# Kernel tuning notes

Measured on AMD Instinct MI355X. Metric: run time of the kernel, lower is better.

Reference implementation:

```python
import jax, jax.numpy as jnp
import numpy as np

N_NODES = 4096
N_EDGES = 32768
IN_FEAT = 256
OUT_FEAT = 128
HID = 64
IN_HEAD = 64
OUT_HEAD = 5
NEG_SLOPE = 0.2
EPS = 1e-16


def setup_inputs() -> dict:
    key = jax.random.key(0)
    ks = jax.random.split(key, 12)
    x = jax.random.normal(ks[0], (N_NODES, IN_FEAT), dtype=jnp.float32)
    src = jax.random.randint(ks[1], (N_EDGES,), 0, N_NODES)
    dst = jax.random.randint(ks[2], (N_EDGES,), 0, N_NODES)
    edge_index = jnp.stack([src, dst]).astype(jnp.int64)
    s1 = 1.0 / np.sqrt(IN_FEAT)
    s2 = 1.0 / np.sqrt(HID * IN_HEAD)
    W1 = jax.random.normal(ks[3], (IN_FEAT, IN_HEAD * HID), dtype=jnp.float32) * s1
    att_src1 = jax.random.normal(ks[4], (IN_HEAD, HID), dtype=jnp.float32) * 0.1
    att_dst1 = jax.random.normal(ks[5], (IN_HEAD, HID), dtype=jnp.float32) * 0.1
    b1 = jnp.zeros((IN_HEAD * HID,), dtype=jnp.float32)
    W2 = jax.random.normal(ks[6], (IN_HEAD * HID, OUT_HEAD * OUT_FEAT), dtype=jnp.float32) * s2
    att_src2 = jax.random.normal(ks[7], (OUT_HEAD, OUT_FEAT), dtype=jnp.float32) * 0.1
    att_dst2 = jax.random.normal(ks[8], (OUT_HEAD, OUT_FEAT), dtype=jnp.float32) * 0.1
    b2 = jnp.zeros((OUT_FEAT,), dtype=jnp.float32)
    return {"x": x, "edge_index": edge_index, "W1": W1, "att_src1": att_src1,
            "att_dst1": att_dst1, "b1": b1, "W2": W2, "att_src2": att_src2,
            "att_dst2": att_dst2, "b2": b2}


def _gat_conv(x, W, att_src, att_dst, bias, src, dst, heads, out_c, concat):
    # x: [N, F_in]; returns [N, heads*out_c] (concat) or [N, out_c] (mean)
    n = x.shape[0]
    h = (x @ W).reshape(n, heads, out_c)                       # [N,H,C]
    a_src = jnp.sum(h * att_src, axis=-1)                      # [N,H]
    a_dst = jnp.sum(h * att_dst, axis=-1)                      # [N,H]
    e = jax.nn.leaky_relu(a_src[src] + a_dst[dst], NEG_SLOPE)  # [E,H]
    # segment softmax over edges grouped by destination node (PyG softmax)
    m = jax.ops.segment_max(e, dst, num_segments=n)            # [N,H]
    ex = jnp.exp(e - m[dst])
    denom = jax.ops.segment_sum(ex, dst, num_segments=n)       # [N,H]
    alpha = ex / (denom[dst] + EPS)                            # [E,H]
    out = jax.ops.segment_sum(alpha[:, :, None] * h[src], dst, num_segments=n)  # [N,H,C]
    out = out.reshape(n, heads * out_c) if concat else out.mean(axis=1)
    return out + bias


def reference(x, edge_index, W1, att_src1, att_dst1, b1, W2, att_src2, att_dst2, b2):
    n = x.shape[0]
    # PyG GATConv default: add self loops
    loop = jnp.arange(n, dtype=edge_index.dtype)
    src = jnp.concatenate([edge_index[0], loop])
    dst = jnp.concatenate([edge_index[1], loop])
    # dropout layers are identity in eval mode
    h = _gat_conv(x, W1, att_src1, att_dst1, b1, src, dst, IN_HEAD, HID, True)
    h = jax.nn.elu(h)
    h = _gat_conv(h, W2, att_src2, att_dst2, b2, src, dst, OUT_HEAD, OUT_FEAT, False)
    s = jnp.mean(h, axis=0)
    return jnp.tanh(s)
```

## Files before the change

kernel.cpp:

```cpp
#include <hip/hip_runtime.h>
#include <hip/hip_bf16.h>

#define N_NODES 4096
#define NE      32768
#define E_TOT   (NE + N_NODES)
#define IN_FEAT 256
#define HID     64
#define IN_HEAD 64
#define F1      4096
#define OUT_HEAD 5
#define OUT_FEAT 128
#define F2      640
#define NEG_SLOPE 0.2f
#define EPS_A   1e-16f

typedef __bf16 bf16;
typedef bf16 bf16x8 __attribute__((ext_vector_type(8)));
typedef bf16 bf16x4 __attribute__((ext_vector_type(4)));
typedef float f32x4 __attribute__((ext_vector_type(4)));

__device__ inline void async_cp16(bf16* lds, const bf16* g) {
    __builtin_amdgcn_global_load_lds(
        (const __attribute__((address_space(1))) unsigned int*)g,
        (__attribute__((address_space(3))) unsigned int*)lds, 16, 0, 0);
}

__global__ void scan_kernel(const int* __restrict__ counts,
                            int* __restrict__ row_start, int* __restrict__ cursor) {
    __shared__ int part[256];
    __shared__ int pre[257];
    int t = threadIdx.x;
    int base = t * 16;
    int local[16];
    int s = 0;
#pragma unroll
    for (int i = 0; i < 16; ++i) { local[i] = s; s += counts[base + i]; }
    part[t] = s;
    __syncthreads();
    if (t == 0) {
        int r = 0;
        for (int i = 0; i < 256; ++i) { pre[i] = r; r += part[i]; }
        pre[256] = r;
    }
    __syncthreads();
    int off = pre[t];
#pragma unroll
    for (int i = 0; i < 16; ++i) {
        int v = off + local[i];
        row_start[base + i] = v;
        cursor[base + i] = v;
    }
    if (t == 0) row_start[N_NODES] = pre[256];
}

__global__ void scatter_kernel(const int* __restrict__ esrc,
                               const int* __restrict__ edst,
                               int* cursor, int* __restrict__ srclist) {
    int e = blockIdx.x * 256 + threadIdx.x;
    if (e >= E_TOT) return;
    int d = (e < NE) ? edst[e] : (e - NE);
    int s = (e < NE) ? esrc[e] : (e - NE);
    int slot = atomicAdd(&cursor[d], 1);
    srclist[slot] = s;
}

#define PB_X   512
#define PB_W1  1024
#define PB_W2  2560
#define PB_ATT 64
#define PB_TOT (PB_X + PB_W1 + PB_W2 + PB_ATT)
#define PB_HIST 144
__global__ __launch_bounds__(256)
void prep_kernel(const float* __restrict__ x, bf16* __restrict__ xb,
                 const float* __restrict__ W1, bf16* __restrict__ W1T,
                 const float* __restrict__ W2, bf16* __restrict__ W2T,
                 const float* __restrict__ as1, const float* __restrict__ ad1,
                 bf16* __restrict__ w1s, bf16* __restrict__ w1d,
                 const int* __restrict__ edst, int* __restrict__ counts) {
    __shared__ float tile[32][33];
    int b = blockIdx.x, t = threadIdx.x;
    if (b < PB_X) {
        int i = b * 256 + t;
        f32x4 a = *(const f32x4*)(x + (size_t)i * 8);
        f32x4 c = *(const f32x4*)(x + (size_t)i * 8 + 4);
        bf16x8 r;
        r[0] = (bf16)a[0]; r[1] = (bf16)a[1]; r[2] = (bf16)a[2]; r[3] = (bf16)a[3];
        r[4] = (bf16)c[0]; r[5] = (bf16)c[1]; r[6] = (bf16)c[2]; r[7] = (bf16)c[3];
        *(bf16x8*)(xb + (size_t)i * 8) = r;
    } else if (b < PB_X + PB_W1 + PB_W2) {
        const float* S; bf16* D; int R, C, gx, gy;
        if (b < PB_X + PB_W1) {
            int bb = b - PB_X;
            S = W1; D = W1T; R = IN_FEAT; C = F1;
            gx = bb % (F1 / 32); gy = bb / (F1 / 32);
        } else {
            int bb = b - PB_X - PB_W1;
            S = W2; D = W2T; R = F1; C = F2;
            gx = bb % (F2 / 32); gy = bb / (F2 / 32);
        }
        int tx = t & 31, ty = t >> 5;
        int c0 = gx * 32, r0 = gy * 32;
#pragma unroll
        for (int i = 0; i < 4; ++i)
            tile[ty + i * 8][tx] = S[(size_t)(r0 + ty + i * 8) * C + c0 + tx];
        __syncthreads();
#pragma unroll
        for (int i = 0; i < 4; ++i)
            D[(size_t)(c0 + ty + i * 8) * R + r0 + tx] = (bf16)tile[tx][ty + i * 8];
    } else if (b < PB_TOT) {
        int id = (b - PB_X - PB_W1 - PB_W2) * 256 + t;
        int k = id >> 6, h = id & 63;
        const float* wrow = W1 + (size_t)k * F1 + h * HID;
        const float* a1 = as1 + h * HID;
        const float* a2 = ad1 + h * HID;
        float s = 0.f, d = 0.f;
#pragma unroll 8
        for (int c = 0; c < HID; ++c) {
            float w = wrow[c];
            s += w * a1[c];
            d += w * a2[c];
        }
        w1s[id] = (bf16)s;
        w1d[id] = (bf16)d;
    } else {
        int e = (b - PB_TOT) * 256 + t;
        if (e < E_TOT) {
            int d = (e < NE) ? edst[e] : (e - NE);
            atomicAdd(&counts[d], 1);
        }
    }
}

template <int SPLITK, typename TC>
__device__ __forceinline__
void gemm_body(const bf16* __restrict__ A, const bf16* __restrict__ BT,
               TC* __restrict__ C, int M, int N, int K,
               int nb, int mb, int zb) {
    __shared__ bf16 As[128][64];
    __shared__ bf16 Bs[128][64];
    const int tid  = threadIdx.x;
    const int wave = tid >> 6, lane = tid & 63;
    const int quad = lane >> 4, lr = lane & 15;
    const int m0 = mb * 128, n0 = nb * 128;
    const int kchunk = K / SPLITK;
    const int kbeg = zb * kchunk;
    const int wm = (wave >> 1) * 64;
    const int wn = (wave & 1) * 64;
    TC* Cz = C + (size_t)zb * M * N;

    const int srow = lane >> 3;
    const int scol = ((lane & 7) ^ srow) * 8;
    const int xk = lr & 7;

    f32x4 acc[4][4] = {};

    for (int kk = 0; kk < kchunk; kk += 64) {
        int k0 = kbeg + kk;
#pragma unroll
        for (int c = 0; c < 4; ++c) {
            int r = wave * 32 + c * 8;
            async_cp16(&As[r][0], A + (size_t)(m0 + r + srow) * K + k0 + scol);
            async_cp16(&Bs[r][0], BT + (size_t)(n0 + r + srow) * K + k0 + scol);
        }
        __syncthreads();

#pragma unroll
        for (int ks = 0; ks < 2; ++ks) {
            int ch = ((ks * 4 + quad) ^ xk) * 8;
            bf16x8 af[4], bfr[4];
#pragma unroll
            for (int mt = 0; mt < 4; ++mt)
                af[mt] = *(const bf16x8*)(&As[wm + mt * 16 + lr][ch]);
#pragma unroll
            for (int nt = 0; nt < 4; ++nt)
                bfr[nt] = *(const bf16x8*)(&Bs[wn + nt * 16 + lr][ch]);
#pragma unroll
            for (int mt = 0; mt < 4; ++mt)
#pragma unroll
                for (int nt = 0; nt < 4; ++nt)
                    acc[mt][nt] = __builtin_amdgcn_mfma_f32_16x16x32_bf16(
                        af[mt], bfr[nt], acc[mt][nt], 0, 0, 0);
        }
        __syncthreads();
    }

#pragma unroll
    for (int mt = 0; mt < 4; ++mt)
#pragma unroll
        for (int nt = 0; nt < 4; ++nt) {
            int row0 = m0 + wm + mt * 16 + quad * 4;
            int col = n0 + wn + nt * 16 + lr;
#pragma unroll
            for (int r = 0; r < 4; ++r)
                Cz[(size_t)(row0 + r) * N + col] = (TC)acc[mt][nt][r];
        }
}

__global__ __launch_bounds__(256)
void gemm2_kernel(const bf16* __restrict__ A, const bf16* __restrict__ BT,
                  bf16* __restrict__ C) {
    int bid = blockIdx.x;
    int xx = bid & 7, q = bid >> 3;
    int gp = q / 5; int nb = q - gp * 5;
    int g = gp * 8 + xx;
    int mb = g >> 2, zb = g & 3;
    gemm_body<4, bf16>(A, BT, C, N_NODES, F2, F1, nb, mb, zb);
}

__global__ __launch_bounds__(256)
void layer1_kernel(const bf16* __restrict__ xb, const bf16* __restrict__ W1T,
                   bf16* __restrict__ H1,
                   const float* __restrict__ x,
                   const bf16* __restrict__ w1s, const bf16* __restrict__ w1d,
                   float* __restrict__ a_src, float* __restrict__ a_dst) {
    int bid = blockIdx.x;
    if (bid < 1024) {
        gemm_body<1, bf16>(xb, W1T, H1, N_NODES, F1, IN_FEAT,
                           bid & 31, bid >> 5, 0);
    } else {
        int wave = threadIdx.x >> 6, lane = threadIdx.x & 63;
        int n = (bid - 1024) * 4 + wave;
        const float* xr = x + (size_t)n * IN_FEAT;
        float s = 0.f, d = 0.f;
        for (int k0 = 0; k0 < IN_FEAT; k0 += 4) {
            f32x4 xv = *(const f32x4*)(xr + k0);
#pragma unroll
            for (int j = 0; j < 4; ++j) {
                float xs = xv[j];
                s += xs * (float)w1s[(k0 + j) * IN_HEAD + lane];
                d += xs * (float)w1d[(k0 + j) * IN_HEAD + lane];
            }
        }
        a_src[n * IN_HEAD + lane] = s;
        a_dst[n * IN_HEAD + lane] = d;
    }
}

__global__ __launch_bounds__(64)
void agg1_kernel(const int* __restrict__ row_start,
                 const int* __restrict__ srclist,
                 const float* __restrict__ a_src, const float* __restrict__ a_dst,
                 const bf16* __restrict__ H1, const float* __restrict__ b1,
                 bf16* __restrict__ h_elu) {
    int bid = blockIdx.x;
    int c = bid & 7;
    int d = bid >> 3;
    int lane = threadIdx.x;
    int gh = c * 8 + (lane >> 3);
    int beg = row_start[d], deg = row_start[d + 1] - beg;
    float adst = a_dst[d * IN_HEAD + gh];
    int fbase = c * 512 + lane * 8;
    const float* asg = a_src + gh;

    auto SL = [&](int i) { return srclist[beg + (i < deg ? i : deg - 1)]; };

    int s0 = SL(0), s1 = SL(1), s2 = SL(2), s3 = SL(3);
    float la0 = asg[(size_t)s0 * IN_HEAD];
    bf16x8 v0 = *(const bf16x8*)(H1 + (size_t)s0 * F1 + fbase);
    float la1 = asg[(size_t)s1 * IN_HEAD];
    bf16x8 v1 = *(const bf16x8*)(H1 + (size_t)s1 * F1 + fbase);
    float la2 = asg[(size_t)s2 * IN_HEAD];
    bf16x8 v2 = *(const bf16x8*)(H1 + (size_t)s2 * F1 + fbase);
    float la3 = asg[(size_t)s3 * IN_HEAD];
    bf16x8 v3 = *(const bf16x8*)(H1 + (size_t)s3 * F1 + fbase);
    int s4 = SL(4), s5 = SL(5);

    float m = -1e30f, den = 0.f;
    float acc[8] = {};
    for (int i = 0; i < deg; ++i) {
        int sn = SL(i + 6);
        float la4 = asg[(size_t)s4 * IN_HEAD];
        bf16x8 v4 = *(const bf16x8*)(H1 + (size_t)s4 * F1 + fbase);

        float l = la0 + adst;
        l = l > 0.f ? l : NEG_SLOPE * l;
        if (l > m + 12.f) {
            float r = __expf(m - l);
            den *= r;
#pragma unroll
            for (int k = 0; k < 8; ++k) acc[k] *= r;
            m = l;
        }
        float w = __expf(l - m);
        den += w;
#pragma unroll
        for (int k = 0; k < 8; ++k) acc[k] += w * (float)v0[k];

        la0 = la1; v0 = v1;
        la1 = la2; v1 = v2;
        la2 = la3; v2 = v3;
        la3 = la4; v3 = v4;
        s4 = s5; s5 = sn;
    }
    float dinv = 1.f / (den + EPS_A);

    bf16x8 o;
#pragma unroll
    for (int j = 0; j < 8; ++j) {
        float v = acc[j] * dinv + b1[fbase + j];
        o[j] = (bf16)(v > 0.f ? v : (__expf(v) - 1.f));
    }
    *(bf16x8*)(h_elu + (size_t)d * F1 + fbase) = o;
}

__global__ __launch_bounds__(192)
void fold2_kernel(const bf16* __restrict__ Hp,
                  const float* __restrict__ as2, const float* __restrict__ ad2,
                  float* __restrict__ H2,
                  float* __restrict__ a_src, float* __restrict__ a_dst) {
    int n = blockIdx.x, t = threadIdx.x;
    if (t >= 160) return;
    int h = t >> 5;
    f32x4 sum = {};
#pragma unroll
    for (int z = 0; z < 4; ++z) {
        bf16x4 v = *(const bf16x4*)(Hp + (size_t)z * N_NODES * F2 + (size_t)n * F2 + t * 4);
        sum[0] += (float)v[0]; sum[1] += (float)v[1];
        sum[2] += (float)v[2]; sum[3] += (float)v[3];
    }
    *(f32x4*)(H2 + (size_t)n * F2 + t * 4) = sum;
    f32x4 ws = *(const f32x4*)(as2 + t * 4);
    f32x4 wd = *(const f32x4*)(ad2 + t * 4);
    float s = sum[0] * ws[0] + sum[1] * ws[1] + sum[2] * ws[2] + sum[3] * ws[3];
    float d = sum[0] * wd[0] + sum[1] * wd[1] + sum[2] * wd[2] + sum[3] * wd[3];
#pragma unroll
    for (int o = 1; o <= 16; o <<= 1) {
        s += __shfl_xor(s, o);
        d += __shfl_xor(d, o);
    }
    if ((t & 31) == 0) {
        a_src[n * OUT_HEAD + h] = s;
        a_dst[n * OUT_HEAD + h] = d;
    }
}

__global__ void stats2_kernel(const int* __restrict__ row_start,
                              const int* __restrict__ srclist,
                              const float* __restrict__ a_src,
                              const float* __restrict__ a_dst,
                              float* __restrict__ m2, float* __restrict__ dinv2,
                              float* __restrict__ beta) {
    int id = blockIdx.x * 256 + threadIdx.x;
    if (id >= N_NODES * OUT_HEAD) return;
    beta[id] = 0.f;
    int d = id / OUT_HEAD, h = id - d * OUT_HEAD;
    int beg = row_start[d], deg = row_start[d + 1] - beg;
    float adst = a_dst[id];
    auto SL = [&](int i) { return srclist[beg + (i < deg ? i : deg - 1)]; };
    int s0 = SL(0), s1 = SL(1);
    float la0 = a_src[s0 * OUT_HEAD + h];
    float m = -1e30f, den = 0.f;
    for (int i = 0; i < deg; ++i) {
        int s2 = SL(i + 2);
        float la1 = a_src[s1 * OUT_HEAD + h];
        float l = la0 + adst;
        l = l > 0.f ? l : NEG_SLOPE * l;
        if (l > m + 12.f) { den *= __expf(m - l); m = l; }
        den += __expf(l - m);
        la0 = la1; s1 = s2;
    }
    m2[id] = m;
    dinv2[id] = 1.f / (den + EPS_A);
}

__global__ void beta_kernel(const int* __restrict__ es, const int* __restrict__ ed,
                            const float* __restrict__ a_src, const float* __restrict__ a_dst,
                            const float* __restrict__ m2, const float* __restrict__ dinv2,
                            float* __restrict__ beta,
                            float* __restrict__ acc_out, int* __restrict__ ticket) {
    int id = blockIdx.x * 256 + threadIdx.x;
    if (id < 8 * OUT_FEAT) acc_out[id] = 0.f;
    else if (id == 8 * OUT_FEAT) *ticket = 0;
    if (id >= E_TOT * OUT_HEAD) return;
    int e = id / OUT_HEAD, h = id - e * OUT_HEAD;
    int s = (e < NE) ? es[e] : (e - NE);
    int d = (e < NE) ? ed[e] : (e - NE);
    float l = a_src[s * OUT_HEAD + h] + a_dst[d * OUT_HEAD + h];
    l = l > 0.f ? l : NEG_SLOPE * l;
    float alpha = __expf(l - m2[d * OUT_HEAD + h]) * dinv2[d * OUT_HEAD + h];
    atomicAdd(&beta[s * OUT_HEAD + h], alpha);
}

__global__ __launch_bounds__(256)
void wsum_kernel(const float* __restrict__ H2, const float* __restrict__ beta,
                 float* __restrict__ acc_out, const float* __restrict__ b2,
                 float* __restrict__ out, int* __restrict__ ticket) {
    __shared__ float buf[F2];
    __shared__ int lastblk;
    int t = threadIdx.x;
    int n0 = blockIdx.x * 32;
    int h = t >> 5;
    float a0 = 0.f, a1 = 0.f, a2 = 0.f, a3 = 0.f;
    if (t < 160) {
        for (int i = 0; i < 32; ++i) {
            int s = n0 + i;
            float bh = beta[s * OUT_HEAD + h];
            f32x4 v = *(const f32x4*)(H2 + (size_t)s * F2 + t * 4);
            a0 += bh * v[0]; a1 += bh * v[1];
            a2 += bh * v[2]; a3 += bh * v[3];
        }
        buf[t * 4 + 0] = a0; buf[t * 4 + 1] = a1;
        buf[t * 4 + 2] = a2; buf[t * 4 + 3] = a3;
    }
    __syncthreads();
    if (t < OUT_FEAT) {
        float s = 0.f;
#pragma unroll
        for (int hh = 0; hh < OUT_HEAD; ++hh) s += buf[hh * OUT_FEAT + t];
        atomicAdd(&acc_out[(blockIdx.x & 7) * OUT_FEAT + t], s);
    }
    __syncthreads();
    if (t == 0) {
        __threadfence();
        lastblk = (atomicAdd(ticket, 1) == (int)gridDim.x - 1);
    }
    __syncthreads();
    if (lastblk && t < OUT_FEAT) {
        float tot = 0.f;
#pragma unroll
        for (int k = 0; k < 8; ++k)
            tot += atomicAdd(&acc_out[k * OUT_FEAT + t], 0.0f);
        out[t] = tanhf(tot * (1.f / (OUT_HEAD * (float)N_NODES)) + b2[t]);
    }
}

extern "C" void kernel_launch(void* const* d_in, const int* in_sizes, int n_in,
                              void* d_out, int out_size, void* d_ws, size_t ws_size,
                              hipStream_t stream) {
    const float* x        = (const float*)d_in[0];
    const int*   ei       = (const int*)d_in[1];
    const float* W1       = (const float*)d_in[2];
    const float* att_src1 = (const float*)d_in[3];
    const float* att_dst1 = (const float*)d_in[4];
    const float* b1       = (const float*)d_in[5];
    const float* W2       = (const float*)d_in[6];
    const float* att_src2 = (const float*)d_in[7];
    const float* att_dst2 = (const float*)d_in[8];
    const float* b2       = (const float*)d_in[9];
    float* out = (float*)d_out;

    const int* esrc = ei;
    const int* edst = ei + NE;

    char* p = (char*)d_ws;
    auto bump = [&](size_t bytes) {
        void* r = (void*)p;
        p += (bytes + 255) & ~(size_t)255;
        return r;
    };
    bf16*  H1     = (bf16*)bump((size_t)N_NODES * F1 * 2);
    bf16*  h_elu  = (bf16*)bump((size_t)N_NODES * F1 * 2);
    bf16*  Hp     = (bf16*)bump((size_t)4 * N_NODES * F2 * 2);
    float* H2     = (float*)bump((size_t)N_NODES * F2 * 4);
    bf16*  xb     = (bf16*)bump((size_t)N_NODES * IN_FEAT * 2);
    bf16*  W1T    = (bf16*)bump((size_t)F1 * IN_FEAT * 2);
    bf16*  W2T    = (bf16*)bump((size_t)F2 * F1 * 2);
    bf16*  w1s    = (bf16*)bump((size_t)IN_FEAT * IN_HEAD * 2);
    bf16*  w1d    = (bf16*)bump((size_t)IN_FEAT * IN_HEAD * 2);
    float* a_src1 = (float*)bump((size_t)N_NODES * IN_HEAD * 4);
    float* a_dst1 = (float*)bump((size_t)N_NODES * IN_HEAD * 4);
    float* a_src2 = (float*)bump((size_t)N_NODES * OUT_HEAD * 4);
    float* a_dst2 = (float*)bump((size_t)N_NODES * OUT_HEAD * 4);
    float* m2     = (float*)bump((size_t)N_NODES * OUT_HEAD * 4);
    float* dinv2  = (float*)bump((size_t)N_NODES * OUT_HEAD * 4);
    int*   row_start = (int*)bump((N_NODES + 1) * 4);
    int*   cursor  = (int*)bump(N_NODES * 4);
    int*   srclist = (int*)bump(E_TOT * 4);
    int*   counts  = (int*)bump(N_NODES * 4);
    float* beta    = (float*)bump((size_t)N_NODES * OUT_HEAD * 4);
    float* acc_out = (float*)bump((size_t)8 * OUT_FEAT * 4);
    int*   ticket  = (int*)bump(4);

    hipMemsetAsync(counts, 0, N_NODES * 4, stream);
    prep_kernel<<<PB_TOT + PB_HIST, 256, 0, stream>>>(
        x, xb, W1, W1T, W2, W2T, att_src1, att_dst1, w1s, w1d, edst, counts);
    scan_kernel<<<1, 256, 0, stream>>>(counts, row_start, cursor);
    scatter_kernel<<<(E_TOT + 255) / 256, 256, 0, stream>>>(
        esrc, edst, cursor, srclist);

    layer1_kernel<<<2048, 256, 0, stream>>>(
        xb, W1T, H1, x, w1s, w1d, a_src1, a_dst1);
    agg1_kernel<<<N_NODES * 8, 64, 0, stream>>>(
        row_start, srclist, a_src1, a_dst1, H1, b1, h_elu);

    gemm2_kernel<<<640, 256, 0, stream>>>(h_elu, W2T, Hp);
    fold2_kernel<<<N_NODES, 192, 0, stream>>>(
        Hp, att_src2, att_dst2, H2, a_src2, a_dst2);
    stats2_kernel<<<(N_NODES * OUT_HEAD + 255) / 256, 256, 0, stream>>>(
        row_start, srclist, a_src2, a_dst2, m2, dinv2, beta);
    beta_kernel<<<(E_TOT * OUT_HEAD + 255) / 256, 256, 0, stream>>>(
        esrc, edst, a_src2, a_dst2, m2, dinv2, beta, acc_out, ticket);
    wsum_kernel<<<N_NODES / 32, 256, 0, stream>>>(
        H2, beta, acc_out, b2, out, ticket);
}
```

Baseline: 238.7 us.

## Split layer-1 GEMM and GEMV into separate kernels with wider GEMM tile

The fused layer1 kernel, which mixed GEMM blocks with attention-logit GEMV blocks, is split into a dedicated gemm1 kernel and a separate gemv1 kernel. The new GEMM uses a 128x256 output tile per block (8 N-subtiles per wave) on a 2D grid, which doubles reuse of the A tile and halves the number of blocks. The wider tile raises accumulator register pressure and LDS use, and adds one more kernel launch. The shared gemm_body template is inlined into each kernel.

Result: slower. 251.3 us (+5.3%).

```diff
diff --git a/kernel.cpp b/kernel.cpp
--- a/kernel.cpp
+++ b/kernel.cpp
@@ -131,109 +131,158 @@
     }
 }
 
-template <int SPLITK, typename TC>
-__device__ __forceinline__
-void gemm_body(const bf16* __restrict__ A, const bf16* __restrict__ BT,
-               TC* __restrict__ C, int M, int N, int K,
-               int nb, int mb, int zb) {
+__global__ __launch_bounds__(256)
+void gemm1_kernel(const bf16* __restrict__ A, const bf16* __restrict__ BT,
+                  bf16* __restrict__ C) {
+    __shared__ bf16 As[128][64];
+    __shared__ bf16 Bs[256][64];
+    const int tid  = threadIdx.x;
+    const int wave = tid >> 6, lane = tid & 63;
+    const int quad = lane >> 4, lr = lane & 15;
+    const int nb = blockIdx.x;
+    const int mb = blockIdx.y;
+    const int m0 = mb * 128, n0 = nb * 256;
+    const int wm = (wave >> 1) * 64;
+    const int wn = (wave & 1) * 128;
+
+    const int srow = lane >> 3;
+    const int scol = ((lane & 7) ^ srow) * 8;
+    const int xk = lr & 7;
+
+    f32x4 acc[4][8] = {};
+
+    for (int k0 = 0; k0 < IN_FEAT; k0 += 64) {
+#pragma unroll
+        for (int c = 0; c < 4; ++c) {
+            int r = wave * 32 + c * 8;
+            async_cp16(&As[r][0], A + (size_t)(m0 + r + srow) * IN_FEAT + k0 + scol);
+        }
+#pragma unroll
+        for (int c = 0; c < 8; ++c) {
+            int r = wave * 64 + c * 8;
+            async_cp16(&Bs[r][0], BT + (size_t)(n0 + r + srow) * IN_FEAT + k0 + scol);
+        }
+        __syncthreads();
+
+#pragma unroll
+        for (int ks = 0; ks < 2; ++ks) {
+            int ch = ((ks * 4 + quad) ^ xk) * 8;
+            bf16x8 af[4], bfr[8];
+#pragma unroll
+            for (int mt = 0; mt < 4; ++mt)
+                af[mt] = *(const bf16x8*)(&As[wm + mt * 16 + lr][ch]);
+#pragma unroll
+            for (int nt = 0; nt < 8; ++nt)
+                bfr[nt] = *(const bf16x8*)(&Bs[wn + nt * 16 + lr][ch]);
+#pragma unroll
+            for (int mt = 0; mt < 4; ++mt)
+#pragma unroll
+                for (int nt = 0; nt < 8; ++nt)
+                    acc[mt][nt] = __builtin_amdgcn_mfma_f32_16x16x32_bf16(
+                        af[mt], bfr[nt], acc[mt][nt], 0, 0, 0);
+        }
+        __syncthreads();
+    }
+
+#pragma unroll
+    for (int mt = 0; mt < 4; ++mt)
+#pragma unroll
+        for (int nt = 0; nt < 8; ++nt) {
+            int row0 = m0 + wm + mt * 16 + quad * 4;
+            int col = n0 + wn + nt * 16 + lr;
+#pragma unroll
+            for (int r = 0; r < 4; ++r)
+                C[(size_t)(row0 + r) * F1 + col] = (bf16)acc[mt][nt][r];
+        }
+}
+
+__global__ __launch_bounds__(256)
+void gemm2_kernel(const bf16* __restrict__ A, const bf16* __restrict__ BT,
+                  bf16* __restrict__ C) {
     __shared__ bf16 As[128][64];
     __shared__ bf16 Bs[128][64];
     const int tid  = threadIdx.x;
     const int wave = tid >> 6, lane = tid & 63;
     const int quad = lane >> 4, lr = lane & 15;
-    const int m0 = mb * 128, n0 = nb * 128;
-    const int kchunk = K / SPLITK;
-    const int kbeg = zb * kchunk;
-    const int wm = (wave >> 1) * 64;
-    const int wn = (wave & 1) * 64;
-    TC* Cz = C + (size_t)zb * M * N;
-
-    const int srow = lane >> 3;
-    const int scol = ((lane & 7) ^ srow) * 8;
-    const int xk = lr & 7;
-
-    f32x4 acc[4][4] = {};
-
-    for (int kk = 0; kk < kchunk; kk += 64) {
-        int k0 = kbeg + kk;
-#pragma unroll
-        for (int c = 0; c < 4; ++c) {
-            int r = wave * 32 + c * 8;
-            async_cp16(&As[r][0], A + (size_t)(m0 + r + srow) * K + k0 + scol);
-            async_cp16(&Bs[r][0], BT + (size_t)(n0 + r + srow) * K + k0 + scol);
-        }
-        __syncthreads();
-
-#pragma unroll
-        for (int ks = 0; ks < 2; ++ks) {
-            int ch = ((ks * 4 + quad) ^ xk) * 8;
-            bf16x8 af[4], bfr[4];
-#pragma unroll
-            for (int mt = 0; mt < 4; ++mt)
-                af[mt] = *(const bf16x8*)(&As[wm + mt * 16 + lr][ch]);
-#pragma unroll
-            for (int nt = 0; nt < 4; ++nt)
-                bfr[nt] = *(const bf16x8*)(&Bs[wn + nt * 16 + lr][ch]);
-#pragma unroll
-            for (int mt = 0; mt < 4; ++mt)
-#pragma unroll
-                for (int nt = 0; nt < 4; ++nt)
-                    acc[mt][nt] = __builtin_amdgcn_mfma_f32_16x16x32_bf16(
-                        af[mt], bfr[nt], acc[mt][nt], 0, 0, 0);
-        }
-        __syncthreads();
-    }
-
-#pragma unroll
-    for (int mt = 0; mt < 4; ++mt)
-#pragma unroll
-        for (int nt = 0; nt < 4; ++nt) {
-            int row0 = m0 + wm + mt * 16 + quad * 4;
-            int col = n0 + wn + nt * 16 + lr;
-#pragma unroll
-            for (int r = 0; r < 4; ++r)
-                Cz[(size_t)(row0 + r) * N + col] = (TC)acc[mt][nt][r];
-        }
-}
-
-__global__ __launch_bounds__(256)
-void gemm2_kernel(const bf16* __restrict__ A, const bf16* __restrict__ BT,
-                  bf16* __restrict__ C) {
     int bid = blockIdx.x;
     int xx = bid & 7, q = bid >> 3;
     int gp = q / 5; int nb = q - gp * 5;
     int g = gp * 8 + xx;
     int mb = g >> 2, zb = g & 3;
-    gemm_body<4, bf16>(A, BT, C, N_NODES, F2, F1, nb, mb, zb);
+    const int m0 = mb * 128, n0 = nb * 128;
+    const int kchunk = F1 / 4;
+    const int kbeg = zb * kchunk;
+    const int wm = (wave >> 1) * 64;
+    const int wn = (wave & 1) * 64;
+    bf16* Cz = C + (size_t)zb * N_NODES * F2;
+
+    const int srow = lane >> 3;
+    const int scol = ((lane & 7) ^ srow) * 8;
+    const int xk = lr & 7;
+
+    f32x4 acc[4][4] = {};
+
+    for (int kk = 0; kk < kchunk; kk += 64) {
+        int k0 = kbeg + kk;
+#pragma unroll
+        for (int c = 0; c < 4; ++c) {
+            int r = wave * 32 + c * 8;
+            async_cp16(&As[r][0], A + (size_t)(m0 + r + srow) * F1 + k0 + scol);
+            async_cp16(&Bs[r][0], BT + (size_t)(n0 + r + srow) * F1 + k0 + scol);
+        }
+        __syncthreads();
+
+#pragma unroll
+        for (int ks = 0; ks < 2; ++ks) {
+            int ch = ((ks * 4 + quad) ^ xk) * 8;
+            bf16x8 af[4], bfr[4];
+#pragma unroll
+            for (int mt = 0; mt < 4; ++mt)
+                af[mt] = *(const bf16x8*)(&As[wm + mt * 16 + lr][ch]);
+#pragma unroll
+            for (int nt = 0; nt < 4; ++nt)
+                bfr[nt] = *(const bf16x8*)(&Bs[wn + nt * 16 + lr][ch]);
+#pragma unroll
+            for (int mt = 0; mt < 4; ++mt)
+#pragma unroll
+                for (int nt = 0; nt < 4; ++nt)
+                    acc[mt][nt] = __builtin_amdgcn_mfma_f32_16x16x32_bf16(
+                        af[mt], bfr[nt], acc[mt][nt], 0, 0, 0);
+        }
+        __syncthreads();
+    }
+
+#pragma unroll
+    for (int mt = 0; mt < 4; ++mt)
+#pragma unroll
+        for (int nt = 0; nt < 4; ++nt) {
+            int row0 = m0 + wm + mt * 16 + quad * 4;
+            int col = n0 + wn + nt * 16 + lr;
+#pragma unroll
+            for (int r = 0; r < 4; ++r)
+                Cz[(size_t)(row0 + r) * F2 + col] = (bf16)acc[mt][nt][r];
+        }
 }
 
 __global__ __launch_bounds__(256)
-void layer1_kernel(const bf16* __restrict__ xb, const bf16* __restrict__ W1T,
-                   bf16* __restrict__ H1,
-                   const float* __restrict__ x,
-                   const bf16* __restrict__ w1s, const bf16* __restrict__ w1d,
-                   float* __restrict__ a_src, float* __restrict__ a_dst) {
-    int bid = blockIdx.x;
-    if (bid < 1024) {
-        gemm_body<1, bf16>(xb, W1T, H1, N_NODES, F1, IN_FEAT,
-                           bid & 31, bid >> 5, 0);
-    } else {
-        int wave = threadIdx.x >> 6, lane = threadIdx.x & 63;
-        int n = (bid - 1024) * 4 + wave;
-        const float* xr = x + (size_t)n * IN_FEAT;
-        float s = 0.f, d = 0.f;
-        for (int k0 = 0; k0 < IN_FEAT; k0 += 4) {
-            f32x4 xv = *(const f32x4*)(xr + k0);
-#pragma unroll
-            for (int j = 0; j < 4; ++j) {
-                float xs = xv[j];
-                s += xs * (float)w1s[(k0 + j) * IN_HEAD + lane];
-                d += xs * (float)w1d[(k0 + j) * IN_HEAD + lane];
-            }
-        }
-        a_src[n * IN_HEAD + lane] = s;
-        a_dst[n * IN_HEAD + lane] = d;
-    }
+void gemv1_kernel(const float* __restrict__ x,
+                  const bf16* __restrict__ w1s, const bf16* __restrict__ w1d,
+                  float* __restrict__ a_src, float* __restrict__ a_dst) {
+    int wave = threadIdx.x >> 6, lane = threadIdx.x & 63;
+    int n = blockIdx.x * 4 + wave;
+    const float* xr = x + (size_t)n * IN_FEAT;
+    float s = 0.f, d = 0.f;
+    for (int k0 = 0; k0 < IN_FEAT; k0 += 4) {
+        f32x4 xv = *(const f32x4*)(xr + k0);
+#pragma unroll
+        for (int j = 0; j < 4; ++j) {
+            float xs = xv[j];
+            s += xs * (float)w1s[(k0 + j) * IN_HEAD + lane];
+            d += xs * (float)w1d[(k0 + j) * IN_HEAD + lane];
+        }
+    }
+    a_src[n * IN_HEAD + lane] = s;
+    a_dst[n * IN_HEAD + lane] = d;
 }
 
 __global__ __launch_bounds__(64)
@@ -478,8 +527,9 @@
     scatter_kernel<<<(E_TOT + 255) / 256, 256, 0, stream>>>(
         esrc, edst, cursor, srclist);
 
-    layer1_kernel<<<2048, 256, 0, stream>>>(
-        xb, W1T, H1, x, w1s, w1d, a_src1, a_dst1);
+    gemm1_kernel<<<dim3(F1 / 256, N_NODES / 128), 256, 0, stream>>>(
+        xb, W1T, H1);
+    gemv1_kernel<<<N_NODES / 4, 256, 0, stream>>>(x, w1s, w1d, a_src1, a_dst1);
     agg1_kernel<<<N_NODES * 8, 64, 0, stream>>>(
         row_start, srclist, a_src1, a_dst1, H1, b1, h_elu);
 
```
